# Performance work log

Hardware: AMD Instinct MI355X
Metric: run time of the kernel (lower is better)

The kernel has to match this reference:

```python
import jax, jax.numpy as jnp
import numpy as np

N_EMBD = 1024
QK_DIM = 16


def setup_inputs() -> dict:
    key = jax.random.key(0)
    k1, k2, k3, k4, k5 = jax.random.split(key, 5)
    b, s = 8, 2048
    lim = 1.0 / np.sqrt(N_EMBD)  # torch Linear default init range
    return {
        "x": jax.random.normal(k1, (b, s, N_EMBD), dtype=jnp.float32),
        "w_q": jax.random.uniform(k2, (QK_DIM, N_EMBD), minval=-lim, maxval=lim, dtype=jnp.float32),
        "b_q": jax.random.uniform(k3, (QK_DIM,), minval=-lim, maxval=lim, dtype=jnp.float32),
        "w_k": jax.random.uniform(k4, (QK_DIM, N_EMBD), minval=-lim, maxval=lim, dtype=jnp.float32),
        "b_k": jax.random.uniform(k5, (QK_DIM,), minval=-lim, maxval=lim, dtype=jnp.float32),
    }


def reference(x, w_q, b_q, w_k, b_k):
    # x: [b, s, d_model]
    s = x.shape[-2]
    q = jnp.einsum("bsd,ed->bse", x, w_q) + b_q  # [b, s, qk_dim]
    k = jnp.einsum("bsd,ed->bse", x, w_k) + b_k  # [b, s, qk_dim]
    scale = 1.0 / jnp.sqrt(jnp.asarray(QK_DIM, dtype=x.dtype))
    mask = jnp.arange(s)[:, None] >= jnp.arange(s)[None, :]  # causal [s, s]
    scores = jnp.einsum("bqe,bke->bqk", q, k) * scale  # [b, s, s]
    scores = jnp.where(mask[None], scores, jnp.asarray(-10000.0, dtype=x.dtype))
    probs = jax.nn.softmax(scores, axis=-1)
    return jnp.einsum("bqk,bkv->bqv", probs, x)  # identity OV: weighted sum of x
```

## Files before the change

### kernel.cpp

```cpp
#include <hip/hip_runtime.h>

typedef __attribute__((ext_vector_type(4))) float  f32x4;
typedef __attribute__((ext_vector_type(8))) short  bf16x8;
typedef __attribute__((ext_vector_type(4))) unsigned int u32x4;

#define MFMA16(a,b,c) __builtin_amdgcn_mfma_f32_16x16x32_bf16(a,b,c,0,0,0)
#define SCL   0.360673760f
#define PBIAS 17.3123405f

static __device__ __forceinline__ unsigned short f2bf(float f){
  unsigned int u = __float_as_uint(f);
  u += 0x7fffu + ((u>>16)&1u);
  return (unsigned short)(u>>16);
}
static __device__ __forceinline__ unsigned int pk2(float a, float b){
  return (unsigned)f2bf(a) | (((unsigned)f2bf(b))<<16);
}
static __device__ __forceinline__ float expfast(float a){
  float e; asm("v_exp_f32 %0, %1" : "=v"(e) : "v"(a)); return e;
}

__global__ __launch_bounds__(256,2) void prep_kernel(
    const float* __restrict__ x,  const float* __restrict__ wq, const float* __restrict__ bq,
    const float* __restrict__ wk, const float* __restrict__ bk,
    unsigned short* __restrict__ qws, unsigned short* __restrict__ kws,
    unsigned char* __restrict__ xpk)
{
  __shared__ __align__(16) unsigned short wlds[32*1032];
  __shared__ __align__(16) unsigned short xlds[64*72];
  const int t  = threadIdx.x;
  const int r0 = blockIdx.x<<6;
  const int b  = r0>>11;
  const int s0 = r0&2047;
  const int l = t&63, w = t>>6, g = l>>4, li = l&15;

  { const int n = t>>3, part = t&7;
    const float* wsrc = (n<16) ? (wq + n*1024) : (wk + (n-16)*1024);
    #pragma unroll
    for(int cc=0; cc<16; ++cc){
      const int d = part*128 + cc*8;
      f32x4 f0 = *(const f32x4*)(wsrc + d);
      f32x4 f1 = *(const f32x4*)(wsrc + d + 4);
      u32x4 p;
      p[0]=pk2(f0[0],f0[1]); p[1]=pk2(f0[2],f0[3]);
      p[2]=pk2(f1[0],f1[1]); p[3]=pk2(f1[2],f1[3]);
      *(u32x4*)(&wlds[n*1032 + d]) = p;
    }
  }
  __syncthreads();

  f32x4 acc0 = {0.f,0.f,0.f,0.f};
  f32x4 acc1 = {0.f,0.f,0.f,0.f};
  const int srow = t>>2, dch = t&3;
  const int dd = t&63, sch = t>>6;

  unsigned char* pdst = xpk + ((size_t)(b*64 + (s0>>5) + (sch>>1)))*65536
                      + (size_t)(dd>>4)*1024 + (size_t)(sch&1)*512 + (size_t)(dd&15)*16;

  for(int it=0; it<16; ++it){
    { const float* xp = x + (size_t)(r0+srow)*1024 + it*64 + dch*16;
      f32x4 a0 = *(const f32x4*)(xp);
      f32x4 a1 = *(const f32x4*)(xp+4);
      f32x4 a2 = *(const f32x4*)(xp+8);
      f32x4 a3 = *(const f32x4*)(xp+12);
      u32x4 p0, p1;
      p0[0]=pk2(a0[0],a0[1]); p0[1]=pk2(a0[2],a0[3]);
      p0[2]=pk2(a1[0],a1[1]); p0[3]=pk2(a1[2],a1[3]);
      p1[0]=pk2(a2[0],a2[1]); p1[1]=pk2(a2[2],a2[3]);
      p1[2]=pk2(a3[0],a3[1]); p1[3]=pk2(a3[2],a3[3]);
      *(u32x4*)(&xlds[srow*72 + dch*16])     = p0;
      *(u32x4*)(&xlds[srow*72 + dch*16 + 8]) = p1;
    }
    __syncthreads();
    #pragma unroll
    for(int ks=0; ks<2; ++ks){
      bf16x8 a  = *(const bf16x8*)(&xlds[(16*w+li)*72       + ks*32 + g*8]);
      bf16x8 b0 = *(const bf16x8*)(&wlds[ li*1032     + it*64 + ks*32 + g*8]);
      bf16x8 b1 = *(const bf16x8*)(&wlds[(16+li)*1032 + it*64 + ks*32 + g*8]);
      acc0 = MFMA16(a,b0,acc0);
      acc1 = MFMA16(a,b1,acc1);
    }
    {
      unsigned short v[16];
      #pragma unroll
      for(int jj=0; jj<16; ++jj) v[jj] = xlds[(sch*16 + jj)*72 + dd];
      u32x4 o0, o1;
      o0[0]=(unsigned)v[0]|((unsigned)v[1]<<16);   o0[1]=(unsigned)v[2]|((unsigned)v[3]<<16);
      o0[2]=(unsigned)v[4]|((unsigned)v[5]<<16);   o0[3]=(unsigned)v[6]|((unsigned)v[7]<<16);
      o1[0]=(unsigned)v[8]|((unsigned)v[9]<<16);   o1[1]=(unsigned)v[10]|((unsigned)v[11]<<16);
      o1[2]=(unsigned)v[12]|((unsigned)v[13]<<16); o1[3]=(unsigned)v[14]|((unsigned)v[15]<<16);
      unsigned char* dst = pdst + (size_t)it*4096;
      *(u32x4*)(dst)       = o0;
      *(u32x4*)(dst + 256) = o1;
    }
    __syncthreads();
  }
  #pragma unroll
  for(int reg=0; reg<4; ++reg){
    const int sr = r0 + 16*w + 4*g + reg;
    qws[(size_t)sr*16 + li] = f2bf(acc0[reg] + bq[li]);
    kws[(size_t)sr*16 + li] = f2bf(acc1[reg] + bk[li]);
  }
}

__global__ __launch_bounds__(256,3) void attn_kernel(
    const unsigned short* __restrict__ qws, const unsigned short* __restrict__ kws,
    const unsigned char* __restrict__ xpk, float* __restrict__ out)
{
  __shared__ __align__(16) unsigned char pshare[8192];
  __shared__ float psL[64];
  const int t = threadIdx.x;
  const int l = t&63, w = t>>6, g = l>>4, li = l&15;
  const int bi = blockIdx.x;
  const int b = bi&7;
  const int j = bi>>3;
  const int qb = 31-(j>>2), dq = j&3;
  const int q0 = qb<<6, d0 = dq<<8, nt = 2*qb + 2;

  const int kperm = ((li>>2)<<3) + (li&3);

  const bf16x8 zero8 = {0,0,0,0,0,0,0,0};
  bf16x8 qfr = zero8;
  if(g < 2) qfr = *(const bf16x8*)(qws + ((size_t)(b*2048 + q0 + 16*w + li)<<4) + 8*g);
  const int qg = q0 + 16*w + li;

  f32x4 acc[4][4];
  #pragma unroll
  for(int i=0;i<4;++i)
    #pragma unroll
    for(int jj=0;jj<4;++jj){ acc[i][jj][0]=0.f; acc[i][jj][1]=0.f; acc[i][jj][2]=0.f; acc[i][jj][3]=0.f; }
  float sp = 0.f;

  const unsigned char* xq = xpk + (size_t)(b*64)*65536 + (size_t)(16*dq + 4*w)*1024 + l*16;
  const unsigned short* kp0 = kws + ((size_t)(b*2048 + kperm)<<4) + 8*g;

  bf16x8 k1 = *(const bf16x8*)(kp0);
  bf16x8 k2 = *(const bf16x8*)(kp0 + 64);
  u32x4 xc[4];
  #pragma unroll
  for(int df=0; df<4; ++df) xc[df] = *(const u32x4*)(xq + df*1024);

  int buf = 0;
  for(int tt=0; tt<nt; ++tt){
    const int kv0 = tt<<5;
    const int tn = (tt+1 < nt) ? tt+1 : tt;
    u32x4 xn[4];
    const unsigned char* xqn = xq + (size_t)tn*65536;
    #pragma unroll
    for(int df=0; df<4; ++df) xn[df] = *(const u32x4*)(xqn + df*1024);
    f32x4 z = {0.f,0.f,0.f,0.f};
    f32x4 s1 = MFMA16(k1, qfr, z);
    f32x4 s2 = MFMA16(k2, qfr, z);
    const unsigned short* kpn = kp0 + (size_t)(tn<<5)*16;
    bf16x8 n1 = *(const bf16x8*)(kpn);
    bf16x8 n2 = *(const bf16x8*)(kpn + 64);
    float p[8];
    if(tt < nt-2){
      #pragma unroll
      for(int r=0;r<4;++r){
        p[r]   = expfast(fmaf(s1[r], SCL, -PBIAS));
        p[4+r] = expfast(fmaf(s2[r], SCL, -PBIAS));
      }
    } else {
      #pragma unroll
      for(int r=0;r<4;++r){
        p[r]   = (kv0 + 8*g + r   <= qg) ? expfast(fmaf(s1[r], SCL, -PBIAS)) : 0.f;
        p[4+r] = (kv0 + 8*g + 4+r <= qg) ? expfast(fmaf(s2[r], SCL, -PBIAS)) : 0.f;
      }
    }
    sp += ((p[0]+p[1])+(p[2]+p[3])) + ((p[4]+p[5])+(p[6]+p[7]));
    { u32x4 av;
      asm("v_cvt_pk_bf16_f32 %0, %1, %2" : "=v"(av[0]) : "v"(p[0]), "v"(p[1]));
      asm("v_cvt_pk_bf16_f32 %0, %1, %2" : "=v"(av[1]) : "v"(p[2]), "v"(p[3]));
      asm("v_cvt_pk_bf16_f32 %0, %1, %2" : "=v"(av[2]) : "v"(p[4]), "v"(p[5]));
      asm("v_cvt_pk_bf16_f32 %0, %1, %2" : "=v"(av[3]) : "v"(p[6]), "v"(p[7]));
      *(u32x4*)(&pshare[buf*4096 + w*1024 + l*16]) = av;
    }
    asm volatile("s_waitcnt lgkmcnt(0)" ::: "memory");
    __builtin_amdgcn_sched_barrier(0);
    __builtin_amdgcn_s_barrier();
    __builtin_amdgcn_sched_barrier(0);
    __builtin_amdgcn_s_setprio(1);
    bf16x8 a0 = *(const bf16x8*)(&pshare[buf*4096 +        l*16]);
    bf16x8 a1 = *(const bf16x8*)(&pshare[buf*4096 + 1024 + l*16]);
    bf16x8 a2 = *(const bf16x8*)(&pshare[buf*4096 + 2048 + l*16]);
    bf16x8 a3 = *(const bf16x8*)(&pshare[buf*4096 + 3072 + l*16]);
    #pragma unroll
    for(int df=0; df<4; ++df){
      bf16x8 bfr = *(const bf16x8*)(&xc[df]);
      acc[0][df] = MFMA16(a0, bfr, acc[0][df]);
      acc[1][df] = MFMA16(a1, bfr, acc[1][df]);
      acc[2][df] = MFMA16(a2, bfr, acc[2][df]);
      acc[3][df] = MFMA16(a3, bfr, acc[3][df]);
    }
    __builtin_amdgcn_s_setprio(0);
    buf ^= 1; k1 = n1; k2 = n2;
    #pragma unroll
    for(int df=0; df<4; ++df) xc[df] = xn[df];
  }

  float r_ = sp;
  r_ += __shfl_xor(r_, 16);
  r_ += __shfl_xor(r_, 32);
  if(l < 16) psL[16*w + l] = r_;
  __syncthreads();
  #pragma unroll
  for(int qf=0; qf<4; ++qf){
    const f32x4 pv = *(const f32x4*)(&psL[16*qf + 4*g]);
    #pragma unroll
    for(int reg=0; reg<4; ++reg){
      const float inv = 1.0f/pv[reg];
      float* op = out + (size_t)(b*2048 + q0 + 16*qf + 4*g + reg)*1024 + d0 + 64*w + li;
      #pragma unroll
      for(int df=0; df<4; ++df) op[df*16] = acc[qf][df][reg]*inv;
    }
  }
}

extern "C" void kernel_launch(void* const* d_in, const int* in_sizes, int n_in,
                              void* d_out, int out_size, void* d_ws, size_t ws_size,
                              hipStream_t stream) {
  (void)in_sizes; (void)n_in; (void)out_size; (void)ws_size;
  const float* x  = (const float*)d_in[0];
  const float* wq = (const float*)d_in[1];
  const float* bq = (const float*)d_in[2];
  const float* wk = (const float*)d_in[3];
  const float* bk = (const float*)d_in[4];
  float* out = (float*)d_out;
  char* ws = (char*)d_ws;
  unsigned short* qws = (unsigned short*)(ws);
  unsigned short* kws = (unsigned short*)(ws + (512<<10));
  unsigned char*  xpk = (unsigned char*)(ws + (2<<20));
  hipLaunchKernelGGL(prep_kernel, dim3(256), dim3(256), 0, stream, x, wq, bq, wk, bk, qws, kws, xpk);
  hipLaunchKernelGGL(attn_kernel, dim3(1024), dim3(256), 0, stream, qws, kws, xpk, out);
}
```

Before: 70.57 us.

## Process 64-key tiles per iteration, halving loop trips and barriers

The attention loop now covers 64 keys per iteration instead of 32. It computes four score MFMAs and writes two P fragments per wave into a doubled LDS buffer, which halves the number of block barriers and loop iterations. The software prefetch of x into registers for the next tile is dropped; both x tiles are loaded at the top of each iteration instead. Fewer barriers cut sync overhead, but x global-load latency is no longer hidden across iterations and register and LDS use rise.

```diff
diff --git a/kernel.cpp b/kernel.cpp
--- a/kernel.cpp
+++ b/kernel.cpp
@@ -107,7 +107,7 @@
     const unsigned short* __restrict__ qws, const unsigned short* __restrict__ kws,
     const unsigned char* __restrict__ xpk, float* __restrict__ out)
 {
-  __shared__ __align__(16) unsigned char pshare[8192];
+  __shared__ __align__(16) unsigned char pshare[16384];
   __shared__ float psL[64];
   const int t = threadIdx.x;
   const int l = t&63, w = t>>6, g = l>>4, li = l&15;
@@ -115,7 +115,7 @@
   const int b = bi&7;
   const int j = bi>>3;
   const int qb = 31-(j>>2), dq = j&3;
-  const int q0 = qb<<6, d0 = dq<<8, nt = 2*qb + 2;
+  const int q0 = qb<<6, d0 = dq<<8, nt = qb + 1;
 
   const int kperm = ((li>>2)<<3) + (li&3);
 
@@ -136,67 +136,80 @@
 
   bf16x8 k1 = *(const bf16x8*)(kp0);
   bf16x8 k2 = *(const bf16x8*)(kp0 + 64);
-  u32x4 xc[4];
-  #pragma unroll
-  for(int df=0; df<4; ++df) xc[df] = *(const u32x4*)(xq + df*1024);
+  bf16x8 k3 = *(const bf16x8*)(kp0 + 512);
+  bf16x8 k4 = *(const bf16x8*)(kp0 + 576);
 
   int buf = 0;
   for(int tt=0; tt<nt; ++tt){
-    const int kv0 = tt<<5;
-    const int tn = (tt+1 < nt) ? tt+1 : tt;
-    u32x4 xn[4];
-    const unsigned char* xqn = xq + (size_t)tn*65536;
-    #pragma unroll
-    for(int df=0; df<4; ++df) xn[df] = *(const u32x4*)(xqn + df*1024);
+    const int kv0 = tt<<6;
+    u32x4 xc[4], xd[4];
+    const unsigned char* xqt = xq + (size_t)(tt*2)*65536;
+    #pragma unroll
+    for(int df=0; df<4; ++df){
+      xc[df] = *(const u32x4*)(xqt + df*1024);
+      xd[df] = *(const u32x4*)(xqt + 65536 + df*1024);
+    }
     f32x4 z = {0.f,0.f,0.f,0.f};
     f32x4 s1 = MFMA16(k1, qfr, z);
     f32x4 s2 = MFMA16(k2, qfr, z);
-    const unsigned short* kpn = kp0 + (size_t)(tn<<5)*16;
+    f32x4 s3 = MFMA16(k3, qfr, z);
+    f32x4 s4 = MFMA16(k4, qfr, z);
+    const int tn = (tt+1 < nt) ? tt+1 : tt;
+    const unsigned short* kpn = kp0 + (size_t)(tn<<6)*16;
     bf16x8 n1 = *(const bf16x8*)(kpn);
     bf16x8 n2 = *(const bf16x8*)(kpn + 64);
-    float p[8];
-    if(tt < nt-2){
+    bf16x8 n3 = *(const bf16x8*)(kpn + 512);
+    bf16x8 n4 = *(const bf16x8*)(kpn + 576);
+    float p[16];
+    if(tt < nt-1){
       #pragma unroll
       for(int r=0;r<4;++r){
-        p[r]   = expfast(fmaf(s1[r], SCL, -PBIAS));
-        p[4+r] = expfast(fmaf(s2[r], SCL, -PBIAS));
+        p[r]    = expfast(fmaf(s1[r], SCL, -PBIAS));
+        p[4+r]  = expfast(fmaf(s2[r], SCL, -PBIAS));
+        p[8+r]  = expfast(fmaf(s3[r], SCL, -PBIAS));
+        p[12+r] = expfast(fmaf(s4[r], SCL, -PBIAS));
       }
     } else {
+      const int b1 = kv0 + 8*g, b2 = kv0 + 32 + 8*g;
       #pragma unroll
       for(int r=0;r<4;++r){
-        p[r]   = (kv0 + 8*g + r   <= qg) ? expfast(fmaf(s1[r], SCL, -PBIAS)) : 0.f;
-        p[4+r] = (kv0 + 8*g + 4+r <= qg) ? expfast(fmaf(s2[r], SCL, -PBIAS)) : 0.f;
+        p[r]    = (b1+r   <= qg) ? expfast(fmaf(s1[r], SCL, -PBIAS)) : 0.f;
+        p[4+r]  = (b1+4+r <= qg) ? expfast(fmaf(s2[r], SCL, -PBIAS)) : 0.f;
+        p[8+r]  = (b2+r   <= qg) ? expfast(fmaf(s3[r], SCL, -PBIAS)) : 0.f;
+        p[12+r] = (b2+4+r <= qg) ? expfast(fmaf(s4[r], SCL, -PBIAS)) : 0.f;
       }
     }
-    sp += ((p[0]+p[1])+(p[2]+p[3])) + ((p[4]+p[5])+(p[6]+p[7]));
-    { u32x4 av;
-      asm("v_cvt_pk_bf16_f32 %0, %1, %2" : "=v"(av[0]) : "v"(p[0]), "v"(p[1]));
-      asm("v_cvt_pk_bf16_f32 %0, %1, %2" : "=v"(av[1]) : "v"(p[2]), "v"(p[3]));
-      asm("v_cvt_pk_bf16_f32 %0, %1, %2" : "=v"(av[2]) : "v"(p[4]), "v"(p[5]));
-      asm("v_cvt_pk_bf16_f32 %0, %1, %2" : "=v"(av[3]) : "v"(p[6]), "v"(p[7]));
-      *(u32x4*)(&pshare[buf*4096 + w*1024 + l*16]) = av;
+    sp += (((p[0]+p[1])+(p[2]+p[3])) + ((p[4]+p[5])+(p[6]+p[7])))
+        + (((p[8]+p[9])+(p[10]+p[11])) + ((p[12]+p[13])+(p[14]+p[15])));
+    { u32x4 avA, avB;
+      asm("v_cvt_pk_bf16_f32 %0, %1, %2" : "=v"(avA[0]) : "v"(p[0]),  "v"(p[1]));
+      asm("v_cvt_pk_bf16_f32 %0, %1, %2" : "=v"(avA[1]) : "v"(p[2]),  "v"(p[3]));
+      asm("v_cvt_pk_bf16_f32 %0, %1, %2" : "=v"(avA[2]) : "v"(p[4]),  "v"(p[5]));
+      asm("v_cvt_pk_bf16_f32 %0, %1, %2" : "=v"(avA[3]) : "v"(p[6]),  "v"(p[7]));
+      asm("v_cvt_pk_bf16_f32 %0, %1, %2" : "=v"(avB[0]) : "v"(p[8]),  "v"(p[9]));
+      asm("v_cvt_pk_bf16_f32 %0, %1, %2" : "=v"(avB[1]) : "v"(p[10]), "v"(p[11]));
+      asm("v_cvt_pk_bf16_f32 %0, %1, %2" : "=v"(avB[2]) : "v"(p[12]), "v"(p[13]));
+      asm("v_cvt_pk_bf16_f32 %0, %1, %2" : "=v"(avB[3]) : "v"(p[14]), "v"(p[15]));
+      *(u32x4*)(&pshare[buf*8192 + w*2048 +        l*16]) = avA;
+      *(u32x4*)(&pshare[buf*8192 + w*2048 + 1024 + l*16]) = avB;
     }
     asm volatile("s_waitcnt lgkmcnt(0)" ::: "memory");
     __builtin_amdgcn_sched_barrier(0);
     __builtin_amdgcn_s_barrier();
     __builtin_amdgcn_sched_barrier(0);
     __builtin_amdgcn_s_setprio(1);
-    bf16x8 a0 = *(const bf16x8*)(&pshare[buf*4096 +        l*16]);
-    bf16x8 a1 = *(const bf16x8*)(&pshare[buf*4096 + 1024 + l*16]);
-    bf16x8 a2 = *(const bf16x8*)(&pshare[buf*4096 + 2048 + l*16]);
-    bf16x8 a3 = *(const bf16x8*)(&pshare[buf*4096 + 3072 + l*16]);
-    #pragma unroll
-    for(int df=0; df<4; ++df){
-      bf16x8 bfr = *(const bf16x8*)(&xc[df]);
-      acc[0][df] = MFMA16(a0, bfr, acc[0][df]);
-      acc[1][df] = MFMA16(a1, bfr, acc[1][df]);
-      acc[2][df] = MFMA16(a2, bfr, acc[2][df]);
-      acc[3][df] = MFMA16(a3, bfr, acc[3][df]);
+    #pragma unroll
+    for(int qf=0; qf<4; ++qf){
+      bf16x8 aA = *(const bf16x8*)(&pshare[buf*8192 + qf*2048 +        l*16]);
+      bf16x8 aB = *(const bf16x8*)(&pshare[buf*8192 + qf*2048 + 1024 + l*16]);
+      #pragma unroll
+      for(int df=0; df<4; ++df){
+        acc[qf][df] = MFMA16(aA, *(const bf16x8*)(&xc[df]), acc[qf][df]);
+        acc[qf][df] = MFMA16(aB, *(const bf16x8*)(&xd[df]), acc[qf][df]);
+      }
     }
     __builtin_amdgcn_s_setprio(0);
-    buf ^= 1; k1 = n1; k2 = n2;
-    #pragma unroll
-    for(int df=0; df<4; ++df) xc[df] = xn[df];
+    buf ^= 1; k1=n1; k2=n2; k3=n3; k4=n4;
   }
 
   float r_ = sp;
```

New measurement: 68.79 us. 1.03x faster.
